# Optimization experiments

Hardware: AMD Instinct MI355X
Metric: run time of the kernel (lower is better)

## Reference

```python
import jax, jax.numpy as jnp
import numpy as np
from jax import lax

B, L, C = 4, 4096, 512
H = 8           # head_num
D = C // H      # head dim = 64
RR = 4          # reduction_ratio -> reducer conv kernel 7, stride 4
KS = 3          # MixFFN depthwise kernel
ER = 4          # expansion ratio -> 2048 channels
EPS = 1e-5      # torch LayerNorm default eps


def _ln(x, g, b):
    # LayerNorm over last axis, affine per-channel
    m = jnp.mean(x, axis=-1, keepdims=True)
    v = jnp.mean(jnp.square(x - m), axis=-1, keepdims=True)
    return (x - m) * lax.rsqrt(v + EPS) * g + b


def setup_inputs() -> dict:
    key = jax.random.key(0)
    ks = jax.random.split(key, 9)
    s = lambda fan: 1.0 / np.sqrt(fan)
    return {
        "x": jax.random.normal(ks[0], (B, L, C), jnp.float32),
        "w_q": jax.random.normal(ks[1], (C, C), jnp.float32) * s(C),
        "w_k": jax.random.normal(ks[2], (C, C), jnp.float32) * s(C),
        "w_v": jax.random.normal(ks[3], (C, C), jnp.float32) * s(C),
        "w_o": jax.random.normal(ks[4], (C, C), jnp.float32) * s(C),
        "w_red": jax.random.normal(ks[5], (C, C, 2 * RR - 1), jnp.float32) * s(C * (2 * RR - 1)),
        "w_ffn1": jax.random.normal(ks[6], (C, C), jnp.float32) * s(C),
        "w_ffn_dw": jax.random.normal(ks[7], (C * ER, 1, KS), jnp.float32) * s(KS),
        "w_ffn2": jax.random.normal(ks[8], (C, C * ER), jnp.float32) * s(C * ER),
        "ln_gamma": jnp.ones((6, C), jnp.float32),
        "ln_beta": jnp.zeros((6, C), jnp.float32),
    }


def reference(x, w_q, w_k, w_v, w_o, w_red, w_ffn1, w_ffn_dw, w_ffn2, ln_gamma, ln_beta):
    # ln indices: 0=ln1(pre-attn), 1=ln(reducer), 2=ln_q, 3=ln_k, 4=ln_v, 5=ln2(pre-ffn)
    residual = x
    h = _ln(x, ln_gamma[0], ln_beta[0])  # B L C

    # --- spatial-reduction for K/V: reflect-pad strided conv + LN ---
    p = (2 * RR - 1) // 2
    hr = jnp.transpose(h, (0, 2, 1))  # B C L
    hr = jnp.pad(hr, ((0, 0), (0, 0), (p, p)), mode="reflect")
    red = lax.conv_general_dilated(hr, w_red, window_strides=(RR,), padding="VALID",
                                   dimension_numbers=("NCH", "OIH", "NCH"))  # B C Lr
    red = jnp.transpose(red, (0, 2, 1))  # B Lr C
    red = _ln(red, ln_gamma[1], ln_beta[1])

    # --- QKV projections + LayerNorms ---
    q = _ln(h @ w_q.T, ln_gamma[2], ln_beta[2])      # B L C
    k = _ln(red @ w_k.T, ln_gamma[3], ln_beta[3])    # B Lr C
    v = _ln(red @ w_v.T, ln_gamma[4], ln_beta[4])    # B Lr C

    Lr = k.shape[1]
    q = q.reshape(B, L, H, D).transpose(0, 2, 1, 3)   # B h L d
    k = k.reshape(B, Lr, H, D).transpose(0, 2, 1, 3)  # B h Lr d
    v = v.reshape(B, Lr, H, D).transpose(0, 2, 1, 3)

    scores = jnp.einsum("bhqd,bhkd->bhqk", q, k) / jnp.sqrt(jnp.float32(D))
    attn = jax.nn.softmax(scores, axis=-1)
    out = jnp.einsum("bhqk,bhkd->bhqd", attn, v)
    out = out.transpose(0, 2, 1, 3).reshape(B, L, C)
    out = out @ w_o.T

    h2 = out + residual
    residual2 = h2
    f = _ln(h2, ln_gamma[5], ln_beta[5])  # B L C

    # --- MixFFN: 1x1 conv -> depthwise reflect conv (groups=C, out=ER*C) -> GELU -> 1x1 conv ---
    f = jnp.transpose(f, (0, 2, 1))  # B C L
    f = jnp.einsum("oi,bil->bol", w_ffn1, f)  # 1x1, C->C
    pk = (KS - 1) // 2
    fp = jnp.pad(f, ((0, 0), (0, 0), (pk, pk)), mode="reflect")
    f = lax.conv_general_dilated(fp, w_ffn_dw, window_strides=(1,), padding="VALID",
                                 dimension_numbers=("NCH", "OIH", "NCH"),
                                 feature_group_count=C)  # B (ER*C) L
    f = jax.nn.gelu(f, approximate=False)  # torch nn.GELU() is exact erf
    f = jnp.einsum("oi,bil->bol", w_ffn2, f)  # 1x1, ER*C->C
    f = jnp.transpose(f, (0, 2, 1))  # B L C

    return f + residual2
```

## Files before the change

kernel.cpp:

```cpp
#include <hip/hip_runtime.h>
#include <math.h>

typedef __attribute__((ext_vector_type(8))) short short8;
typedef __attribute__((ext_vector_type(4))) float f32x4;
typedef unsigned short u16;
typedef unsigned int u32;
typedef unsigned long long u64;

namespace {
constexpr int kB = 4;
constexpr int kL = 4096;
constexpr int kC = 512;
constexpr int kH = 8;
constexpr int kLr = 1024;
constexpr int kCH = 2048;
constexpr int kKred = 3584;
constexpr float kEps = 1e-5f;
}

__device__ __forceinline__ float bf2f(u16 u) { return __uint_as_float(((u32)u) << 16); }
__device__ __forceinline__ u16 f2bf(float f) {
  u32 u = __float_as_uint(f);
  u32 r = (u + 0x7fffu + ((u >> 16) & 1u)) >> 16;
  return (u16)r;
}
__device__ __forceinline__ u32 cvtpk(float lo, float hi) {
  u32 r;
  asm("v_cvt_pk_bf16_f32 %0, %1, %2" : "=v"(r) : "v"(lo), "v"(hi));
  return r;
}

__device__ __forceinline__ void gload_lds16(const void* g, void* l) {
  __builtin_amdgcn_global_load_lds(
      (const __attribute__((address_space(1))) unsigned int*)g,
      (__attribute__((address_space(3))) unsigned int*)l, 16, 0, 0);
}

__device__ __forceinline__ short8 ldsfrag(const u16* base, int row, int col16) {
  return *(const short8*)(base + (size_t)(((row << 3) + (col16 ^ (row & 7))) << 3));
}

__global__ __launch_bounds__(256) void cvt_weights_kernel(
    const float* __restrict__ w_q, const float* __restrict__ w_k,
    const float* __restrict__ w_v, const float* __restrict__ w_o,
    const float* __restrict__ w_f1, const float* __restrict__ w_f2,
    u16* __restrict__ dst) {
  const int i = (blockIdx.x * 256 + threadIdx.x) * 4;
  const int seg = i >> 18;
  const float* src;
  int off;
  if (seg < 5) {
    src = (seg == 0) ? w_q : (seg == 1) ? w_k : (seg == 2) ? w_v : (seg == 3) ? w_o : w_f1;
    off = i & 262143;
  } else {
    src = w_f2;
    off = i - 1310720;
  }
  const float4 v = *(const float4*)(src + off);
  u16 o[4] = {f2bf(v.x), f2bf(v.y), f2bf(v.z), f2bf(v.w)};
  *(u64*)(dst + i) = *(u64*)o;
}

__global__ __launch_bounds__(256) void repack_wred_kernel(const float* __restrict__ src,
                                                          u16* __restrict__ dst) {
  const int idx = blockIdx.x * 256 + threadIdx.x;
  if (idx >= kC * kKred) return;
  const int o = idx / kKred;
  const int rem = idx - o * kKred;
  const int t = rem >> 9;
  const int i = rem & (kC - 1);
  dst[idx] = f2bf(src[(size_t)(o * kC + i) * 7 + t]);
}

__global__ __launch_bounds__(256) void ln_bf16_kernel(const float* __restrict__ in,
                                                      u16* __restrict__ out,
                                                      const float* __restrict__ g,
                                                      const float* __restrict__ be) {
  const int row = blockIdx.x;
  const int tid = threadIdx.x;
  const float2 v = *(const float2*)(in + (size_t)row * kC + tid * 2);
  float s = v.x + v.y;
  float ss = v.x * v.x + v.y * v.y;
#pragma unroll
  for (int off = 32; off > 0; off >>= 1) {
    s += __shfl_down(s, off);
    ss += __shfl_down(ss, off);
  }
  __shared__ float wsum[4][2];
  __shared__ float mi[2];
  const int wave = tid >> 6, lane = tid & 63;
  if (lane == 0) { wsum[wave][0] = s; wsum[wave][1] = ss; }
  __syncthreads();
  if (tid == 0) {
    const float S = wsum[0][0] + wsum[1][0] + wsum[2][0] + wsum[3][0];
    const float SS = wsum[0][1] + wsum[1][1] + wsum[2][1] + wsum[3][1];
    const float mean = S * (1.0f / kC);
    const float var = SS * (1.0f / kC) - mean * mean;
    mi[0] = mean;
    mi[1] = rsqrtf(var + kEps);
  }
  __syncthreads();
  const float mean = mi[0], inv = mi[1];
  const float2 gg = *(const float2*)(g + tid * 2);
  const float2 bb = *(const float2*)(be + tid * 2);
  u16 o2[2] = {f2bf((v.x - mean) * inv * gg.x + bb.x), f2bf((v.y - mean) * inv * gg.y + bb.y)};
  *(u32*)(out + (size_t)row * kC + tid * 2) = *(u32*)o2;
}

__global__ __launch_bounds__(256) void reduce2_ln_kernel(const float* __restrict__ P,
                                                         u16* __restrict__ out,
                                                         const float* __restrict__ g,
                                                         const float* __restrict__ be) {
  const int row = blockIdx.x;
  const int tid = threadIdx.x;
  const size_t stride = (size_t)kB * kLr * kC;
  float2 v = make_float2(0.f, 0.f);
#pragma unroll
  for (int z = 0; z < 2; ++z) {
    const float2 p = *(const float2*)(P + z * stride + (size_t)row * kC + tid * 2);
    v.x += p.x;
    v.y += p.y;
  }
  float s = v.x + v.y;
  float ss = v.x * v.x + v.y * v.y;
#pragma unroll
  for (int off = 32; off > 0; off >>= 1) {
    s += __shfl_down(s, off);
    ss += __shfl_down(ss, off);
  }
  __shared__ float wsum[4][2];
  __shared__ float mi[2];
  const int wave = tid >> 6, lane = tid & 63;
  if (lane == 0) { wsum[wave][0] = s; wsum[wave][1] = ss; }
  __syncthreads();
  if (tid == 0) {
    const float S = wsum[0][0] + wsum[1][0] + wsum[2][0] + wsum[3][0];
    const float SS = wsum[0][1] + wsum[1][1] + wsum[2][1] + wsum[3][1];
    const float mean = S * (1.0f / kC);
    const float var = SS * (1.0f / kC) - mean * mean;
    mi[0] = mean;
    mi[1] = rsqrtf(var + kEps);
  }
  __syncthreads();
  const float mean = mi[0], inv = mi[1];
  const float2 gg = *(const float2*)(g + tid * 2);
  const float2 bb = *(const float2*)(be + tid * 2);
  u16 o2[2] = {f2bf((v.x - mean) * inv * gg.x + bb.x), f2bf((v.y - mean) * inv * gg.y + bb.y)};
  *(u32*)(out + (size_t)row * kC + tid * 2) = *(u32*)o2;
}

__global__ __launch_bounds__(256) void dwgelu_kernel(const u16* __restrict__ f1,
                                                     const float* __restrict__ wdw,
                                                     u16* __restrict__ fdw) {
  const int row = blockIdx.x;
  const int l = row & (kL - 1);
  const int rb = row - l;
  const int cc0 = threadIdx.x * 8;
  const int cg = cc0 >> 2;
  const int lm = (l == 0) ? 1 : l - 1;
  const int lp = (l == kL - 1) ? kL - 2 : l + 1;
  const u32 xm = *(const u32*)(f1 + (size_t)(rb + lm) * kC + cg);
  const u32 x0 = *(const u32*)(f1 + (size_t)(rb + l) * kC + cg);
  const u32 xp = *(const u32*)(f1 + (size_t)(rb + lp) * kC + cg);
  const float xml = bf2f((u16)xm), xmh = bf2f((u16)(xm >> 16));
  const float x0l = bf2f((u16)x0), x0h = bf2f((u16)(x0 >> 16));
  const float xpl = bf2f((u16)xp), xph = bf2f((u16)(xp >> 16));
  float wv[24];
#pragma unroll
  for (int t = 0; t < 6; ++t)
    *(float4*)&wv[t * 4] = *(const float4*)(wdw + (size_t)cc0 * 3 + t * 4);
  short8 pk;
#pragma unroll
  for (int j = 0; j < 8; ++j) {
    const float a_ = (j < 4) ? xml : xmh;
    const float b_ = (j < 4) ? x0l : x0h;
    const float c_ = (j < 4) ? xpl : xph;
    const float dw = wv[j * 3] * a_ + wv[j * 3 + 1] * b_ + wv[j * 3 + 2] * c_;
    pk[j] = (short)f2bf(0.5f * dw * (1.0f + erff(dw * 0.70710678118654752440f)));
  }
  *(short8*)(fdw + (size_t)row * kCH + cc0) = pk;
}

__global__ __launch_bounds__(256) void mgemm_red_kernel(
    const u16* __restrict__ A, const u16* __restrict__ W, float* __restrict__ OutF,
    int M, int N, int K) {
  __shared__ __align__(16) u16 As[2][128 * 64];
  __shared__ __align__(16) u16 Bs[2][128 * 64];
  const int tid = threadIdx.x;
  const int lane = tid & 63, w = tid >> 6;
  const int m0 = blockIdx.y * 128, n0 = blockIdx.x * 128;
  const int wm = (w >> 1) * 64, wn = (w & 1) * 64;
  const f32x4 zero = {0.f, 0.f, 0.f, 0.f};
  f32x4 acc[4][4];
#pragma unroll
  for (int i = 0; i < 4; ++i)
#pragma unroll
    for (int j = 0; j < 4; ++j) acc[i][j] = zero;

  const int kc = K / gridDim.z;
  const int kBeg = blockIdx.z * kc;
  float* outp = OutF + (size_t)blockIdx.z * M * N;

  auto stage = [&](int buf, int k0) {
#pragma unroll
    for (int c = 0; c < 4; ++c) {
      const int ci = w * 4 + c;
      const int idx = ci * 64 + lane;
      const int row = idx >> 3, s = idx & 7;
      const int c16 = s ^ (row & 7);
      gload_lds16(W + (size_t)(n0 + row) * K + k0 + c16 * 8, (char*)Bs[buf] + ci * 1024);
      const int m = m0 + row;
      const int b = m >> 10, lr = m & (kLr - 1);
      const int k = k0 + c16 * 8;
      const int t = k >> 9, i = k & (kC - 1);
      int pos = 4 * lr + t - 3;
      pos = pos < 0 ? -pos : (pos >= kL ? 2 * kL - 2 - pos : pos);
      gload_lds16(A + ((size_t)(b << 12) + pos) * kC + i, (char*)As[buf] + ci * 1024);
    }
  };

  const int nk = kc >> 6;
  stage(0, kBeg);
  __syncthreads();
  for (int t = 0; t < nk; ++t) {
    const int cur = t & 1;
    if (t + 1 < nk) stage(cur ^ 1, kBeg + ((t + 1) << 6));
#pragma unroll
    for (int kst = 0; kst < 2; ++kst) {
      short8 af[4], bfr[4];
      const int c16 = kst * 4 + (lane >> 4);
#pragma unroll
      for (int mb = 0; mb < 4; ++mb) af[mb] = ldsfrag(As[cur], wm + mb * 16 + (lane & 15), c16);
#pragma unroll
      for (int nb = 0; nb < 4; ++nb) bfr[nb] = ldsfrag(Bs[cur], wn + nb * 16 + (lane & 15), c16);
#pragma unroll
      for (int mb = 0; mb < 4; ++mb)
#pragma unroll
        for (int nb = 0; nb < 4; ++nb)
          acc[mb][nb] = __builtin_amdgcn_mfma_f32_16x16x32_bf16(af[mb], bfr[nb], acc[mb][nb], 0, 0, 0);
    }
    __syncthreads();
  }
#pragma unroll
  for (int mb = 0; mb < 4; ++mb)
#pragma unroll
    for (int r = 0; r < 4; ++r) {
      const int row = m0 + wm + mb * 16 + ((lane >> 4) << 2) + r;
#pragma unroll
      for (int nb = 0; nb < 4; ++nb)
        outp[(size_t)row * N + n0 + wn + nb * 16 + (lane & 15)] = acc[mb][nb][r];
    }
}

__global__ __launch_bounds__(256) void mgemm_res_kernel(
    const u16* __restrict__ A, const u16* __restrict__ W,
    const float* __restrict__ Res, float* __restrict__ OutF, int M, int N, int K) {
  __shared__ __align__(16) u16 As[2][128 * 64];
  __shared__ __align__(16) u16 Bs[2][128 * 64];
  const int tid = threadIdx.x;
  const int lane = tid & 63, w = tid >> 6;
  const int m0 = blockIdx.y * 128, n0 = blockIdx.x * 128;
  const int wm = (w >> 1) * 64, wn = (w & 1) * 64;
  const f32x4 zero = {0.f, 0.f, 0.f, 0.f};
  f32x4 acc[4][4];
#pragma unroll
  for (int i = 0; i < 4; ++i)
#pragma unroll
    for (int j = 0; j < 4; ++j) acc[i][j] = zero;

  auto stage = [&](int buf, int k0) {
#pragma unroll
    for (int c = 0; c < 4; ++c) {
      const int ci = w * 4 + c;
      const int idx = ci * 64 + lane;
      const int row = idx >> 3, s = idx & 7;
      const int c16 = s ^ (row & 7);
      gload_lds16(W + (size_t)(n0 + row) * K + k0 + c16 * 8, (char*)Bs[buf] + ci * 1024);
      gload_lds16(A + (size_t)(m0 + row) * K + k0 + c16 * 8, (char*)As[buf] + ci * 1024);
    }
  };

  const int nk = K >> 6;
  stage(0, 0);
  __syncthreads();
  for (int t = 0; t < nk; ++t) {
    const int cur = t & 1;
    if (t + 1 < nk) stage(cur ^ 1, (t + 1) << 6);
#pragma unroll
    for (int kst = 0; kst < 2; ++kst) {
      short8 af[4], bfr[4];
      const int c16 = kst * 4 + (lane >> 4);
#pragma unroll
      for (int mb = 0; mb < 4; ++mb) af[mb] = ldsfrag(As[cur], wm + mb * 16 + (lane & 15), c16);
#pragma unroll
      for (int nb = 0; nb < 4; ++nb) bfr[nb] = ldsfrag(Bs[cur], wn + nb * 16 + (lane & 15), c16);
#pragma unroll
      for (int mb = 0; mb < 4; ++mb)
#pragma unroll
        for (int nb = 0; nb < 4; ++nb)
          acc[mb][nb] = __builtin_amdgcn_mfma_f32_16x16x32_bf16(af[mb], bfr[nb], acc[mb][nb], 0, 0, 0);
    }
    __syncthreads();
  }
#pragma unroll
  for (int mb = 0; mb < 4; ++mb)
#pragma unroll
    for (int r = 0; r < 4; ++r) {
      const int row = m0 + wm + mb * 16 + ((lane >> 4) << 2) + r;
#pragma unroll
      for (int nb = 0; nb < 4; ++nb) {
        const size_t off = (size_t)row * N + n0 + wn + nb * 16 + (lane & 15);
        OutF[off] = acc[mb][nb][r] + Res[off];
      }
    }
}

template <int EPI>
__global__ __launch_bounds__(512) void gemm512_kernel(
    const u16* __restrict__ A, const u16* __restrict__ W,
    const float* __restrict__ Res, float* __restrict__ OutF,
    u16* __restrict__ OutB, u16* __restrict__ OutB2,
    int K, const float* __restrict__ gam, const float* __restrict__ bet, float oscale) {
  constexpr bool RES_ = (EPI == 3);
  constexpr bool LN_ = (EPI == 1 || EPI == 2 || EPI == 3);
  __shared__ __align__(16) u16 As[2][64 * 64];
  __shared__ __align__(16) u16 Bs[2][512 * 64];
  const int tid = threadIdx.x;
  const int lane = tid & 63, w = tid >> 6;
  const int l15 = lane & 15, g = lane >> 4;
  const int m0 = blockIdx.y * 64;
  const int n0 = blockIdx.x * 512;
  const int wn = w << 6;
  const f32x4 zero = {0.f, 0.f, 0.f, 0.f};
  f32x4 acc[4][4];
#pragma unroll
  for (int i = 0; i < 4; ++i)
#pragma unroll
    for (int j = 0; j < 4; ++j) acc[i][j] = zero;

  auto stage = [&](int buf, int k0) {
#pragma unroll
    for (int c = 0; c < 8; ++c) {
      const int cg = (w << 3) + c;
      const int idx = (cg << 6) + lane;
      const int row = idx >> 3, sl = idx & 7;
      const int c16 = sl ^ (row & 7);
      gload_lds16(W + (size_t)(n0 + row) * K + k0 + (c16 << 3), (char*)Bs[buf] + cg * 1024);
    }
    const int idx = (w << 6) + lane;
    const int row = idx >> 3, sl = idx & 7;
    const int c16 = sl ^ (row & 7);
    gload_lds16(A + (size_t)(m0 + row) * K + k0 + (c16 << 3), (char*)As[buf] + w * 1024);
  };

  const int nk = K >> 6;
  stage(0, 0);
  __syncthreads();
  for (int t = 0; t < nk; ++t) {
    const int cur = t & 1;
    if (t + 1 < nk) stage(cur ^ 1, (t + 1) << 6);
#pragma unroll
    for (int kst = 0; kst < 2; ++kst) {
      const int c16 = (kst << 2) + g;
      short8 af[4], bfr[4];
#pragma unroll
      for (int mb = 0; mb < 4; ++mb) af[mb] = ldsfrag(As[cur], (mb << 4) + l15, c16);
#pragma unroll
      for (int nb = 0; nb < 4; ++nb) bfr[nb] = ldsfrag(Bs[cur], wn + (nb << 4) + l15, c16);
#pragma unroll
      for (int mb = 0; mb < 4; ++mb)
#pragma unroll
        for (int nb = 0; nb < 4; ++nb)
          acc[mb][nb] = __builtin_amdgcn_mfma_f32_16x16x32_bf16(af[mb], bfr[nb], acc[mb][nb], 0, 0, 0);
    }
    __syncthreads();
  }

  if (RES_) {
#pragma unroll
    for (int mb = 0; mb < 4; ++mb)
#pragma unroll
      for (int r = 0; r < 4; ++r) {
        const int grow = m0 + (mb << 4) + (g << 2) + r;
#pragma unroll
        for (int nb = 0; nb < 4; ++nb)
          acc[mb][nb][r] += Res[(size_t)grow * kC + wn + (nb << 4) + l15];
      }
  }
  float* rs = (float*)As[0];
  float* rs2 = rs + 512;
  float2* minv = (float2*)(rs2 + 512);
  if (LN_) {
#pragma unroll
    for (int mb = 0; mb < 4; ++mb)
#pragma unroll
      for (int r = 0; r < 4; ++r) {
        float s = acc[mb][0][r] + acc[mb][1][r] + acc[mb][2][r] + acc[mb][3][r];
        float s2 = acc[mb][0][r] * acc[mb][0][r] + acc[mb][1][r] * acc[mb][1][r] +
                   acc[mb][2][r] * acc[mb][2][r] + acc[mb][3][r] * acc[mb][3][r];
        s += __shfl_xor(s, 1); s += __shfl_xor(s, 2); s += __shfl_xor(s, 4); s += __shfl_xor(s, 8);
        s2 += __shfl_xor(s2, 1); s2 += __shfl_xor(s2, 2); s2 += __shfl_xor(s2, 4); s2 += __shfl_xor(s2, 8);
        if (l15 == 0) {
          const int row = (mb << 4) + (g << 2) + r;
          rs[(w << 6) + row] = s;
          rs2[(w << 6) + row] = s2;
        }
      }
    __syncthreads();
    if (tid < 64) {
      float S = 0.f, SS = 0.f;
#pragma unroll
      for (int w8 = 0; w8 < 8; ++w8) { S += rs[(w8 << 6) + tid]; SS += rs2[(w8 << 6) + tid]; }
      const float mean = S * (1.0f / 512.0f);
      const float var = SS * (1.0f / 512.0f) - mean * mean;
      minv[tid] = make_float2(mean, rsqrtf(var + kEps));
    }
    __syncthreads();
  }
  float g4[4], b4[4];
  if (LN_) {
    const float* gp = (EPI == 2 && blockIdx.x) ? gam + kC : gam;
    const float* bp = (EPI == 2 && blockIdx.x) ? bet + kC : bet;
#pragma unroll
    for (int nb = 0; nb < 4; ++nb) {
      const int cc = wn + (nb << 4) + l15;
      g4[nb] = gp[cc];
      b4[nb] = bp[cc];
    }
  }
#pragma unroll
  for (int mb = 0; mb < 4; ++mb) {
#pragma unroll
    for (int r = 0; r < 4; ++r) {
      const int row = (mb << 4) + (g << 2) + r;
      const int grow = m0 + row;
      float2 mi = make_float2(0.f, 0.f);
      if (LN_) mi = minv[row];
#pragma unroll
      for (int nb = 0; nb < 4; ++nb) {
        const int cc = wn + (nb << 4) + l15;
        const float vv = acc[mb][nb][r];
        if (EPI == 0) {
          OutB[(size_t)grow * kC + cc] = f2bf(vv);
        } else if (EPI == 1) {
          OutB[(size_t)grow * kC + cc] = f2bf(((vv - mi.x) * mi.y * g4[nb] + b4[nb]) * oscale);
        } else if (EPI == 2) {
          const float lv = (vv - mi.x) * mi.y * g4[nb] + b4[nb];
          if (blockIdx.x == 0) {
            OutB[(size_t)grow * kC + cc] = f2bf(lv);
          } else {
            const int b = grow >> 10, lr = grow & (kLr - 1);
            const int hh = cc >> 6, d = cc & 63;
            OutB2[((size_t)((b << 3) + hh) * 64 + d) * kLr + lr] = f2bf(lv);
          }
        } else {
          OutF[(size_t)grow * kC + cc] = vv;
          OutB[(size_t)grow * kC + cc] = f2bf((vv - mi.x) * mi.y * g4[nb] + b4[nb]);
        }
      }
    }
  }
}

__global__ __launch_bounds__(256) void attn_mfma_kernel(
    const u16* __restrict__ q, const u16* __restrict__ k,
    const u16* __restrict__ vt, u16* __restrict__ o) {
  __shared__ __align__(16) u16 Qs[64 * 64];
  __shared__ __align__(16) u16 Ks[2][64 * 64];
  __shared__ __align__(16) u16 Vs[2][64 * 64];
  __shared__ __align__(16) u16 Ps[4][16 * 64];
  const int tid = threadIdx.x;
  const int lane = tid & 63, w = tid >> 6;
  const int qt = blockIdx.x, h = blockIdx.y, b = blockIdx.z;
  const int q0 = qt << 6;
  const int l15 = lane & 15, g = lane >> 4;

#pragma unroll
  for (int c = 0; c < 2; ++c) {
    const int ci = (w << 1) + c;
    const int a16 = (ci << 6) + lane;
    const int r = a16 >> 3, sl = a16 & 7;
    gload_lds16(q + (size_t)((b << 12) + q0 + r) * kC + (h << 6) + ((sl ^ (r & 7)) << 3),
                (char*)Qs + ci * 1024);
  }
#pragma unroll
  for (int c = 0; c < 2; ++c) {
    const int ci = (w << 1) + c;
    const int a16 = (ci << 6) + lane;
    const int r = a16 >> 3, sl = a16 & 7;
    const int c16 = sl ^ (r & 7);
    gload_lds16(k + (size_t)((b << 10) + r) * kC + (h << 6) + (c16 << 3), (char*)Ks[0] + ci * 1024);
    gload_lds16(vt + (size_t)(((b << 3) + h) * 64 + r) * kLr + (c16 << 3), (char*)Vs[0] + ci * 1024);
  }

  const f32x4 zero = {0.f, 0.f, 0.f, 0.f};
  float m1 = -1e30f, l1 = 0.f;
  f32x4 accO[4] = {zero, zero, zero, zero};

  __syncthreads();

  for (int t = 0; t < kLr / 64; ++t) {
    const int cur = t & 1;
    if (t < kLr / 64 - 1) {
      const int kv0 = (t + 1) << 6;
#pragma unroll
      for (int c = 0; c < 2; ++c) {
        const int ci = (w << 1) + c;
        const int a16 = (ci << 6) + lane;
        const int r = a16 >> 3, sl = a16 & 7;
        const int c16 = sl ^ (r & 7);
        gload_lds16(k + (size_t)((b << 10) + kv0 + r) * kC + (h << 6) + (c16 << 3),
                    (char*)Ks[cur ^ 1] + ci * 1024);
        gload_lds16(vt + (size_t)(((b << 3) + h) * 64 + r) * kLr + kv0 + (c16 << 3),
                    (char*)Vs[cur ^ 1] + ci * 1024);
      }
    }
    f32x4 st[4] = {zero, zero, zero, zero};
    __builtin_amdgcn_s_setprio(1);
#pragma unroll
    for (int kst = 0; kst < 2; ++kst) {
      const int c16 = (kst << 2) + g;
      const short8 bq = ldsfrag(Qs, (w << 4) + l15, c16);
#pragma unroll
      for (int nb = 0; nb < 4; ++nb) {
        const short8 ak = ldsfrag(Ks[cur], (nb << 4) + l15, c16);
        st[nb] = __builtin_amdgcn_mfma_f32_16x16x32_bf16(ak, bq, st[nb], 0, 0, 0);
      }
    }
    __builtin_amdgcn_s_setprio(0);
    {
      float pm = -1e30f;
#pragma unroll
      for (int nb = 0; nb < 4; ++nb)
#pragma unroll
        for (int r = 0; r < 4; ++r) pm = fmaxf(pm, st[nb][r]);
      pm = fmaxf(pm, __shfl_xor(pm, 16));
      pm = fmaxf(pm, __shfl_xor(pm, 32));
      const bool sk = __all(pm - m1 <= 8.0f);
      float scl = 1.0f;
      if (!sk) {
        const float mnew = fmaxf(m1, pm);
        scl = __expf(m1 - mnew);
        m1 = mnew;
      }
      float ps = 0.f;
#pragma unroll
      for (int nb = 0; nb < 4; ++nb)
#pragma unroll
        for (int r = 0; r < 4; ++r) {
          const float e = __expf(st[nb][r] - m1);
          st[nb][r] = e;
          ps += e;
        }
      ps += __shfl_xor(ps, 16);
      ps += __shfl_xor(ps, 32);
      l1 = l1 * scl + ps;
      char* pw = (char*)&Ps[w][0];
#pragma unroll
      for (int nb = 0; nb < 4; ++nb) {
        const u32 lo = cvtpk(st[nb][0], st[nb][1]);
        const u32 hi = cvtpk(st[nb][2], st[nb][3]);
        const int slot = ((nb << 1) + (g >> 1)) ^ (l15 & 7);
        *(u64*)(pw + (l15 << 7) + (slot << 4) + ((g & 1) << 3)) = ((u64)hi << 32) | lo;
      }
      if (!sk) {
        float scA[4];
#pragma unroll
        for (int r = 0; r < 4; ++r) scA[r] = __shfl(scl, (g << 2) + r);
#pragma unroll
        for (int d = 0; d < 4; ++d)
#pragma unroll
          for (int r = 0; r < 4; ++r) accO[d][r] *= scA[r];
      }
    }
    __builtin_amdgcn_s_setprio(1);
#pragma unroll
    for (int kvs = 0; kvs < 2; ++kvs) {
      const int c16 = (kvs << 2) + g;
      const short8 ap = ldsfrag(&Ps[w][0], l15, c16);
#pragma unroll
      for (int d = 0; d < 4; ++d) {
        const short8 bv = ldsfrag(Vs[cur], (d << 4) + l15, c16);
        accO[d] = __builtin_amdgcn_mfma_f32_16x16x32_bf16(ap, bv, accO[d], 0, 0, 0);
      }
    }
    __builtin_amdgcn_s_setprio(0);
    __syncthreads();
  }
  float li[4];
#pragma unroll
  for (int r = 0; r < 4; ++r) li[r] = 1.0f / __shfl(l1, (g << 2) + r);
  const int qg = (b << 12) + q0 + (w << 4) + (g << 2);
#pragma unroll
  for (int d = 0; d < 4; ++d)
#pragma unroll
    for (int r = 0; r < 4; ++r)
      o[(size_t)(qg + r) * kC + (h << 6) + (d << 4) + l15] = f2bf(accO[d][r] * li[r]);
}

extern "C" void kernel_launch(void* const* d_in, const int* in_sizes, int n_in,
                              void* d_out, int out_size, void* d_ws, size_t ws_size,
                              hipStream_t stream) {
  const float* x      = (const float*)d_in[0];
  const float* w_q    = (const float*)d_in[1];
  const float* w_k    = (const float*)d_in[2];
  const float* w_v    = (const float*)d_in[3];
  const float* w_o    = (const float*)d_in[4];
  const float* w_red  = (const float*)d_in[5];
  const float* w_ffn1 = (const float*)d_in[6];
  const float* w_dw   = (const float*)d_in[7];
  const float* w_ffn2 = (const float*)d_in[8];
  const float* gam    = (const float*)d_in[9];
  const float* bet    = (const float*)d_in[10];
  float* out = (float*)d_out;

  const size_t nBLC = (size_t)kB * kL * kC;
  const size_t nBLrC = (size_t)kB * kLr * kC;
  u16* us = (u16*)d_ws;
  u16* wqb   = us;
  u16* wkb   = wqb + 262144;
  u16* wob   = wkb + 2 * 262144;
  u16* wf1b  = wob + 262144;
  u16* wf2b  = wf1b + 262144;
  u16* wredb = wf2b + 1048576;
  u16* h_b   = wredb + 1835008;
  u16* q_b   = h_b + nBLC;
  u16* red_b = q_b + nBLC;
  u16* k_b   = red_b + nBLrC;
  u16* vt_b  = k_b + nBLrC;
  float* S   = (float*)(vt_b + nBLrC);
  u16* fdw   = q_b;

  cvt_weights_kernel<<<2304, 256, 0, stream>>>(w_q, w_k, w_v, w_o, w_ffn1, w_ffn2, wqb);
  repack_wred_kernel<<<7168, 256, 0, stream>>>(w_red, wredb);

  ln_bf16_kernel<<<kB * kL, 256, 0, stream>>>(x, h_b, gam, bet);
  mgemm_red_kernel<<<dim3(4, 32, 2), 256, 0, stream>>>(h_b, wredb, S, kB * kLr, kC, kKred);
  reduce2_ln_kernel<<<kB * kLr, 256, 0, stream>>>(S, red_b, gam + kC, bet + kC);
  gemm512_kernel<1><<<dim3(1, 256), 512, 0, stream>>>(
      h_b, wqb, nullptr, nullptr, q_b, nullptr, kC, gam + 2 * kC, bet + 2 * kC, 0.125f);
  gemm512_kernel<2><<<dim3(2, 64), 512, 0, stream>>>(
      red_b, wkb, nullptr, nullptr, k_b, vt_b, kC, gam + 3 * kC, bet + 3 * kC, 1.0f);
  attn_mfma_kernel<<<dim3(kL / 64, kH, kB), 256, 0, stream>>>(q_b, k_b, vt_b, h_b);
  gemm512_kernel<3><<<dim3(1, 256), 512, 0, stream>>>(
      h_b, wob, x, out, q_b, nullptr, kC, gam + 5 * kC, bet + 5 * kC, 1.0f);
  gemm512_kernel<0><<<dim3(1, 256), 512, 0, stream>>>(
      q_b, wf1b, nullptr, nullptr, h_b, nullptr, kC, nullptr, nullptr, 1.0f);
  dwgelu_kernel<<<kB * kL, 256, 0, stream>>>(h_b, w_dw, fdw);
  mgemm_res_kernel<<<dim3(4, 128), 256, 0, stream>>>(fdw, wf2b, out, out, kB * kL, kC, kCH);
}
```

Measured before the change: 308.4 us.

## Prefetch two stages ahead with vmcnt waits; hold Q in registers; use exp2 softmax

Result: slower. 319.8 us (+3.7%).

```diff
diff --git a/kernel.cpp b/kernel.cpp
--- a/kernel.cpp
+++ b/kernel.cpp
@@ -17,6 +17,10 @@
 constexpr int kKred = 3584;
 constexpr float kEps = 1e-5f;
 }
+
+#define WAIT_VM(n) asm volatile("s_waitcnt vmcnt(" #n ")" ::: "memory")
+#define WAIT_LGKM0 asm volatile("s_waitcnt lgkmcnt(0)" ::: "memory")
+#define BARRIER_SB() do { __builtin_amdgcn_s_barrier(); __builtin_amdgcn_sched_barrier(0); } while (0)
 
 __device__ __forceinline__ float bf2f(u16 u) { return __uint_as_float(((u32)u) << 16); }
 __device__ __forceinline__ u16 f2bf(float f) {
@@ -221,10 +225,11 @@
 
   const int nk = kc >> 6;
   stage(0, kBeg);
-  __syncthreads();
+  stage(1, kBeg + 64);
   for (int t = 0; t < nk; ++t) {
     const int cur = t & 1;
-    if (t + 1 < nk) stage(cur ^ 1, kBeg + ((t + 1) << 6));
+    if (t + 1 < nk) WAIT_VM(8); else WAIT_VM(0);
+    BARRIER_SB();
 #pragma unroll
     for (int kst = 0; kst < 2; ++kst) {
       short8 af[4], bfr[4];
@@ -239,7 +244,9 @@
         for (int nb = 0; nb < 4; ++nb)
           acc[mb][nb] = __builtin_amdgcn_mfma_f32_16x16x32_bf16(af[mb], bfr[nb], acc[mb][nb], 0, 0, 0);
     }
-    __syncthreads();
+    WAIT_LGKM0;
+    BARRIER_SB();
+    if (t + 2 < nk) stage(cur, kBeg + ((t + 2) << 6));
   }
 #pragma unroll
   for (int mb = 0; mb < 4; ++mb)
@@ -282,10 +289,11 @@
 
   const int nk = K >> 6;
   stage(0, 0);
-  __syncthreads();
+  stage(1, 64);
   for (int t = 0; t < nk; ++t) {
     const int cur = t & 1;
-    if (t + 1 < nk) stage(cur ^ 1, (t + 1) << 6);
+    if (t + 1 < nk) WAIT_VM(8); else WAIT_VM(0);
+    BARRIER_SB();
 #pragma unroll
     for (int kst = 0; kst < 2; ++kst) {
       short8 af[4], bfr[4];
@@ -300,7 +308,9 @@
         for (int nb = 0; nb < 4; ++nb)
           acc[mb][nb] = __builtin_amdgcn_mfma_f32_16x16x32_bf16(af[mb], bfr[nb], acc[mb][nb], 0, 0, 0);
     }
-    __syncthreads();
+    WAIT_LGKM0;
+    BARRIER_SB();
+    if (t + 2 < nk) stage(cur, (t + 2) << 6);
   }
 #pragma unroll
   for (int mb = 0; mb < 4; ++mb)
@@ -355,10 +365,11 @@
 
   const int nk = K >> 6;
   stage(0, 0);
-  __syncthreads();
+  stage(1, 64);
   for (int t = 0; t < nk; ++t) {
     const int cur = t & 1;
-    if (t + 1 < nk) stage(cur ^ 1, (t + 1) << 6);
+    if (t + 1 < nk) WAIT_VM(9); else WAIT_VM(0);
+    BARRIER_SB();
 #pragma unroll
     for (int kst = 0; kst < 2; ++kst) {
       const int c16 = (kst << 2) + g;
@@ -373,7 +384,9 @@
         for (int nb = 0; nb < 4; ++nb)
           acc[mb][nb] = __builtin_amdgcn_mfma_f32_16x16x32_bf16(af[mb], bfr[nb], acc[mb][nb], 0, 0, 0);
     }
-    __syncthreads();
+    WAIT_LGKM0;
+    BARRIER_SB();
+    if (t + 2 < nk) stage(cur, (t + 2) << 6);
   }
 
   if (RES_) {
@@ -465,7 +478,6 @@
 __global__ __launch_bounds__(256) void attn_mfma_kernel(
     const u16* __restrict__ q, const u16* __restrict__ k,
     const u16* __restrict__ vt, u16* __restrict__ o) {
-  __shared__ __align__(16) u16 Qs[64 * 64];
   __shared__ __align__(16) u16 Ks[2][64 * 64];
   __shared__ __align__(16) u16 Vs[2][64 * 64];
   __shared__ __align__(16) u16 Ps[4][16 * 64];
@@ -475,56 +487,48 @@
   const int q0 = qt << 6;
   const int l15 = lane & 15, g = lane >> 4;
 
-#pragma unroll
-  for (int c = 0; c < 2; ++c) {
-    const int ci = (w << 1) + c;
-    const int a16 = (ci << 6) + lane;
-    const int r = a16 >> 3, sl = a16 & 7;
-    gload_lds16(q + (size_t)((b << 12) + q0 + r) * kC + (h << 6) + ((sl ^ (r & 7)) << 3),
-                (char*)Qs + ci * 1024);
-  }
-#pragma unroll
-  for (int c = 0; c < 2; ++c) {
-    const int ci = (w << 1) + c;
-    const int a16 = (ci << 6) + lane;
-    const int r = a16 >> 3, sl = a16 & 7;
-    const int c16 = sl ^ (r & 7);
-    gload_lds16(k + (size_t)((b << 10) + r) * kC + (h << 6) + (c16 << 3), (char*)Ks[0] + ci * 1024);
-    gload_lds16(vt + (size_t)(((b << 3) + h) * 64 + r) * kLr + (c16 << 3), (char*)Vs[0] + ci * 1024);
-  }
+  short8 qf[2];
+#pragma unroll
+  for (int kst = 0; kst < 2; ++kst)
+    qf[kst] = *(const short8*)(q + (size_t)((b << 12) + q0 + (w << 4) + l15) * kC +
+                               (h << 6) + kst * 32 + g * 8);
+
+  auto stageKV = [&](int buf, int t) {
+    const int kv0 = t << 6;
+#pragma unroll
+    for (int c = 0; c < 2; ++c) {
+      const int ci = (w << 1) + c;
+      const int a16 = (ci << 6) + lane;
+      const int r = a16 >> 3, sl = a16 & 7;
+      const int c16 = sl ^ (r & 7);
+      gload_lds16(k + (size_t)((b << 10) + kv0 + r) * kC + (h << 6) + (c16 << 3),
+                  (char*)Ks[buf] + ci * 1024);
+      gload_lds16(vt + (size_t)(((b << 3) + h) * 64 + r) * kLr + kv0 + (c16 << 3),
+                  (char*)Vs[buf] + ci * 1024);
+    }
+  };
+
+  stageKV(0, 0);
+  stageKV(1, 1);
 
   const f32x4 zero = {0.f, 0.f, 0.f, 0.f};
   float m1 = -1e30f, l1 = 0.f;
   f32x4 accO[4] = {zero, zero, zero, zero};
-
-  __syncthreads();
-
-  for (int t = 0; t < kLr / 64; ++t) {
+  constexpr int nt = kLr / 64;
+
+  for (int t = 0; t < nt; ++t) {
     const int cur = t & 1;
-    if (t < kLr / 64 - 1) {
-      const int kv0 = (t + 1) << 6;
-#pragma unroll
-      for (int c = 0; c < 2; ++c) {
-        const int ci = (w << 1) + c;
-        const int a16 = (ci << 6) + lane;
-        const int r = a16 >> 3, sl = a16 & 7;
-        const int c16 = sl ^ (r & 7);
-        gload_lds16(k + (size_t)((b << 10) + kv0 + r) * kC + (h << 6) + (c16 << 3),
-                    (char*)Ks[cur ^ 1] + ci * 1024);
-        gload_lds16(vt + (size_t)(((b << 3) + h) * 64 + r) * kLr + kv0 + (c16 << 3),
-                    (char*)Vs[cur ^ 1] + ci * 1024);
-      }
-    }
+    if (t + 1 < nt) WAIT_VM(4); else WAIT_VM(0);
+    BARRIER_SB();
     f32x4 st[4] = {zero, zero, zero, zero};
     __builtin_amdgcn_s_setprio(1);
 #pragma unroll
     for (int kst = 0; kst < 2; ++kst) {
       const int c16 = (kst << 2) + g;
-      const short8 bq = ldsfrag(Qs, (w << 4) + l15, c16);
 #pragma unroll
       for (int nb = 0; nb < 4; ++nb) {
         const short8 ak = ldsfrag(Ks[cur], (nb << 4) + l15, c16);
-        st[nb] = __builtin_amdgcn_mfma_f32_16x16x32_bf16(ak, bq, st[nb], 0, 0, 0);
+        st[nb] = __builtin_amdgcn_mfma_f32_16x16x32_bf16(ak, qf[kst], st[nb], 0, 0, 0);
       }
     }
     __builtin_amdgcn_s_setprio(0);
@@ -536,11 +540,11 @@
         for (int r = 0; r < 4; ++r) pm = fmaxf(pm, st[nb][r]);
       pm = fmaxf(pm, __shfl_xor(pm, 16));
       pm = fmaxf(pm, __shfl_xor(pm, 32));
-      const bool sk = __all(pm - m1 <= 8.0f);
+      const bool sk = __all(pm - m1 <= 11.5f);
       float scl = 1.0f;
       if (!sk) {
         const float mnew = fmaxf(m1, pm);
-        scl = __expf(m1 - mnew);
+        scl = exp2f(m1 - mnew);
         m1 = mnew;
       }
       float ps = 0.f;
@@ -548,7 +552,7 @@
       for (int nb = 0; nb < 4; ++nb)
 #pragma unroll
         for (int r = 0; r < 4; ++r) {
-          const float e = __expf(st[nb][r] - m1);
+          const float e = exp2f(st[nb][r] - m1);
           st[nb][r] = e;
           ps += e;
         }
@@ -585,7 +589,9 @@
       }
     }
     __builtin_amdgcn_s_setprio(0);
-    __syncthreads();
+    WAIT_LGKM0;
+    BARRIER_SB();
+    if (t + 2 < nt) stageKV(cur, t + 2);
   }
   float li[4];
 #pragma unroll
@@ -638,7 +644,8 @@
   mgemm_red_kernel<<<dim3(4, 32, 2), 256, 0, stream>>>(h_b, wredb, S, kB * kLr, kC, kKred);
   reduce2_ln_kernel<<<kB * kLr, 256, 0, stream>>>(S, red_b, gam + kC, bet + kC);
   gemm512_kernel<1><<<dim3(1, 256), 512, 0, stream>>>(
-      h_b, wqb, nullptr, nullptr, q_b, nullptr, kC, gam + 2 * kC, bet + 2 * kC, 0.125f);
+      h_b, wqb, nullptr, nullptr, q_b, nullptr, kC, gam + 2 * kC, bet + 2 * kC,
+      0.125f * 1.44269504088896f);
   gemm512_kernel<2><<<dim3(2, 64), 512, 0, stream>>>(
       red_b, wkb, nullptr, nullptr, k_b, vt_b, kC, gam + 3 * kC, bet + 3 * kC, 1.0f);
   attn_mfma_kernel<<<dim3(kL / 64, kH, kB), 256, 0, stream>>>(q_b, k_b, vt_b, h_b);
```
